# Kernel optimization log

Hardware: AMD Instinct MI355X
Metric: run time of the kernel (lower is better)

Reference implementation:

```python
import jax, jax.numpy as jnp
import numpy as np

N, K, D_IN, D_OUT = 50000, 32, 128, 128
TEMPERATURE = 1.0


def setup_inputs() -> dict:
    key = jax.random.key(0)
    k1, k2, k3 = jax.random.split(key, 3)
    feat = jax.random.normal(k1, (N, D_IN), dtype=jnp.float32)
    # Glorot-like scale so pairwise distances stay in a reasonable softmax range
    weight = jax.random.normal(k2, (D_IN, D_OUT), dtype=jnp.float32) / np.sqrt(D_IN)
    bias = jnp.zeros((D_OUT,), dtype=jnp.float32)
    # norm='none' -> unit edge weights; fixed-degree-k graph -> topk returns all k neighbors
    top_k_weights = jnp.ones((N, K), dtype=jnp.float32)
    top_k_idx = jax.random.randint(k3, (N, K), 0, N, dtype=jnp.int64)
    return {"feat": feat, "weight": weight, "bias": bias,
            "top_k_weights": top_k_weights, "top_k_idx": top_k_idx}


def reference(feat, weight, bias, top_k_weights, top_k_idx):
    # Linear projection (self.weight): [n, d_out]
    h = feat @ weight
    # Gather top-k neighbor embeddings: [n, k, d]
    fk = h[top_k_idx]
    mask = top_k_idx == -1                      # [n, k] missing-neighbor mask
    w = jnp.where(mask, 0.0, top_k_weights)     # zero out missing weights

    # Pairwise Euclidean distances among each node's k neighbors: [n, k, k]
    # ||a-b|| = sqrt(|a|^2 + |b|^2 - 2 a.b); avoids materializing [n,k,k,d]
    sq = jnp.sum(fk * fk, axis=-1)                          # [n, k]
    gram = jnp.einsum('nkd,nmd->nkm', fk, fk)               # [n, k, k]
    d2 = sq[:, :, None] + sq[:, None, :] - 2.0 * gram
    d2 = jnp.maximum(d2, 0.0)
    dist = jnp.sqrt(jnp.where(d2 > 0.0, d2, 1.0))
    dist = jnp.where(d2 > 0.0, dist, 0.0)                   # zero for identical pts / -1 idx
    # zero entries for missing pairs (matches partial_distance_matrix semantics)
    pair_mask = mask[:, :, None] | mask[:, None, :]
    dist = jnp.where(pair_mask, 0.0, dist)

    # Weighted sum of distances over neighbors (medoid cost): [n, k]
    dagg = jnp.einsum('nm,nkm->nk', w, dist)
    big = jnp.finfo(dist.dtype).max
    dagg = jnp.where(mask | ~jnp.isfinite(dagg), big, dagg)

    # Soft medoid weights
    r = jax.nn.softmax(-dagg / TEMPERATURE, axis=-1)
    # with_weight_correction=True
    r = r * w
    r = r / jnp.sum(r, axis=-1, keepdims=True)
    r = jnp.where(mask, 0.0, r)

    # spmm over the reliable adjacency: [n, d_out]
    out = jnp.einsum('nk,nkd->nd', r, fk)
    return out + bias
```

## Files before the change

kernel.cpp:

```cpp
#include <hip/hip_runtime.h>
#include <math.h>


typedef __attribute__((ext_vector_type(2)))  _Float16 half2v;
typedef __attribute__((ext_vector_type(4)))  _Float16 half4v;
typedef __attribute__((ext_vector_type(8)))  _Float16 half8;
typedef __attribute__((ext_vector_type(16))) float    f32x16;

#define NK   32
#define DIM  128
#define FKT_SZ 4224

__global__ __launch_bounds__(256) void prep(const float* __restrict__ W,
                                            _Float16* __restrict__ WT) {
    int t  = blockIdx.x * 256 + threadIdx.x;
    int nn = t >> 7, k = t & 127;
    WT[t] = (_Float16)W[k * 128 + nn];
}

__global__ __launch_bounds__(64) void gemm128(
    const float* __restrict__ A, const _Float16* __restrict__ WT,
    _Float16* __restrict__ Hq, int n)
{
    const int lane = threadIdx.x;
    const int l31  = lane & 31;
    const int hf   = lane >> 5;

    const int row  = blockIdx.x * 32 + l31;
    const int rowc = row < n ? row : n - 1;

    f32x16 acc[4];
#pragma unroll
    for (int t = 0; t < 4; ++t)
#pragma unroll
        for (int i = 0; i < 16; ++i) acc[t][i] = 0.0f;

    const float* ap = A + (size_t)rowc * 128 + 8 * hf;
#pragma unroll
    for (int s = 0; s < 8; ++s) {
        float4 b0 = *reinterpret_cast<const float4*>(ap + 16 * s);
        float4 b1 = *reinterpret_cast<const float4*>(ap + 16 * s + 4);
        half8 bf;
        bf[0] = (_Float16)b0.x; bf[1] = (_Float16)b0.y;
        bf[2] = (_Float16)b0.z; bf[3] = (_Float16)b0.w;
        bf[4] = (_Float16)b1.x; bf[5] = (_Float16)b1.y;
        bf[6] = (_Float16)b1.z; bf[7] = (_Float16)b1.w;
#pragma unroll
        for (int t = 0; t < 4; ++t) {
            half8 af = *reinterpret_cast<const half8*>(
                WT + (size_t)(l31 + 32 * t) * 128 + 16 * s + 8 * hf);
            acc[t] = __builtin_amdgcn_mfma_f32_32x32x16_f16(af, bf, acc[t], 0, 0, 0);
        }
    }

    if (row < n) {
        _Float16* hp = Hq + (size_t)row * 128;
#pragma unroll
        for (int t = 0; t < 4; ++t)
#pragma unroll
            for (int g = 0; g < 4; ++g) {
                half4v hv;
#pragma unroll
                for (int q = 0; q < 4; ++q) hv[q] = (_Float16)acc[t][4 * g + q];
                *reinterpret_cast<half4v*>(hp + 32 * t + 8 * g + 4 * hf) = hv;
            }
    }
}

__global__ __launch_bounds__(64, 4) void softk(
    const _Float16* __restrict__ hq, const float* __restrict__ bias,
    const float* __restrict__ tkw, const int* __restrict__ idx,
    float* __restrict__ out, int n)
{
    __shared__ __align__(16) _Float16 fkT[FKT_SZ];
    __shared__ __align__(16) float    rbuf[NK];

    const int lane = threadIdx.x;
    const int l31  = lane & 31;
    const int hf   = lane >> 5;
    const int pbase = (lane & 32) + ((lane & 32) >> 3);

    const int d0 = 2 * lane;
    const float2 bv = *reinterpret_cast<const float2*>(bias + d0);
    const _Float16* fb = &fkT[((d0 >> 3) * 33) * 8 + (d0 & 7)];
    const float4* rb = reinterpret_cast<const float4*>(&rbuf[0]);

    const int stride = gridDim.x;
    int nd = blockIdx.x;
    if (nd >= n) return;

    int   vid = idx[(size_t)nd * NK + l31];
    float tw  = tkw[(size_t)nd * NK + l31];
    int   mkc = (vid < 0) ? 1 : 0;
    float wc  = mkc ? 0.0f : tw;
    half8 frag[8];
    {
        const int idr = mkc ? 0 : vid;
        const half8* bp = reinterpret_cast<const half8*>(hq + (size_t)idr * DIM);
#pragma unroll
        for (int s = 0; s < 8; ++s) frag[s] = bp[2 * s + hf];
    }

    while (true) {
        const int  ndn = nd + stride;
        const bool hn  = ndn < n;

        int vid_n = 0; float tw_n = 0.0f;
        if (hn) {
            vid_n = idx[(size_t)ndn * NK + l31];
            tw_n  = tkw[(size_t)ndn * NK + l31];
        }

#pragma unroll
        for (int s = 0; s < 8; ++s) {
            int c = 2 * s + hf;
            *reinterpret_cast<half8*>(&fkT[(c * 33 + l31) * 8]) = frag[s];
        }

        f32x16 acc;
#pragma unroll
        for (int i = 0; i < 16; ++i) acc[i] = 0.0f;
#pragma unroll
        for (int s = 0; s < 8; ++s)
            acc = __builtin_amdgcn_mfma_f32_32x32x16_f16(frag[s], frag[s], acc, 0, 0, 0);

        float sqp = 0.0f;
#pragma unroll
        for (int s = 0; s < 8; ++s) {
            const half2v* p2 = reinterpret_cast<const half2v*>(&frag[s]);
#pragma unroll
            for (int q = 0; q < 4; ++q)
                sqp = __builtin_amdgcn_fdot2(p2[q], p2[q], sqp, false);
        }
        float sq = sqp + __shfl_xor(sqp, 32, 64);

        const int mk_n = (vid_n < 0) ? 1 : 0;
        half8 frag_n[8];
        if (hn) {
            const int idr_n = mk_n ? 0 : vid_n;
            const half8* bpn = reinterpret_cast<const half8*>(hq + (size_t)idr_n * DIM);
#pragma unroll
            for (int s = 0; s < 8; ++s) frag_n[s] = bpn[2 * s + hf];
        }

        {
            _Float16 shi = (_Float16)sq;
            _Float16 slo = (_Float16)(sq - (float)shi);
            _Float16 nh  = (_Float16)(-0.5f * (float)shi);
            _Float16 nl  = (_Float16)(-0.5f * (float)slo);
            _Float16 z   = (_Float16)0.0f, one = (_Float16)1.0f;
            half8 aext = {z, z, z, z, z, z, z, z};
            half8 bext = {z, z, z, z, z, z, z, z};
            if (hf == 0) {
                aext[0] = nh;  aext[1] = nl;  aext[2] = one; aext[3] = one;
                bext[0] = one; bext[1] = one; bext[2] = nh;  bext[3] = nl;
            }
            acc = __builtin_amdgcn_mfma_f32_32x32x16_f16(aext, bext, acc, 0, 0, 0);
        }

        float pt[4] = {0.0f, 0.0f, 0.0f, 0.0f};
#pragma unroll
        for (int reg = 0; reg < 16; ++reg) {
            const int c = (reg & 3) + 8 * (reg >> 2);
            float wr = __shfl(wc, pbase + c, 64);
            float d2 = fmaxf(-(acc[reg] + acc[reg]), 0.0f);
            float ds = (d2 > 1e-4f) ? __builtin_amdgcn_sqrtf(d2) : 0.0f;
            pt[reg & 3] = fmaf(wr, ds, pt[reg & 3]);
        }
        float part = (pt[0] + pt[1]) + (pt[2] + pt[3]);
        float sA = part + __shfl_xor(part, 32, 64);
        if (mkc || !(sA < 3.4028235e38f)) sA = 3.4028235e38f;

        float x  = -sA;
        float mx = x;
#pragma unroll
        for (int o = 16; o > 0; o >>= 1) mx = fmaxf(mx, __shfl_xor(mx, o, 32));
        float t  = __expf(x - mx) * wc;
        float st = t;
#pragma unroll
        for (int o = 16; o > 0; o >>= 1) st += __shfl_xor(st, o, 32);
        float r = t * __builtin_amdgcn_rcpf(st);

        rbuf[l31] = r;

        float o0 = 0.0f, o1 = 0.0f;
#pragma unroll
        for (int q = 0; q < 8; ++q) {
            float4 rv = rb[q];
            half2v h0 = *reinterpret_cast<const half2v*>(fb + 8 * (4 * q + 0));
            half2v h1 = *reinterpret_cast<const half2v*>(fb + 8 * (4 * q + 1));
            half2v h2 = *reinterpret_cast<const half2v*>(fb + 8 * (4 * q + 2));
            half2v h3 = *reinterpret_cast<const half2v*>(fb + 8 * (4 * q + 3));
            o0 = fmaf(rv.x, (float)h0[0], o0); o1 = fmaf(rv.x, (float)h0[1], o1);
            o0 = fmaf(rv.y, (float)h1[0], o0); o1 = fmaf(rv.y, (float)h1[1], o1);
            o0 = fmaf(rv.z, (float)h2[0], o0); o1 = fmaf(rv.z, (float)h2[1], o1);
            o0 = fmaf(rv.w, (float)h3[0], o0); o1 = fmaf(rv.w, (float)h3[1], o1);
        }
        float2 ov = { o0 + bv.x, o1 + bv.y };
        *reinterpret_cast<float2*>(out + (size_t)nd * DIM + d0) = ov;

        if (!hn) break;
        nd  = ndn;
        mkc = mk_n;
        wc  = mk_n ? 0.0f : tw_n;
#pragma unroll
        for (int s = 0; s < 8; ++s) frag[s] = frag_n[s];
    }
}

extern "C" void kernel_launch(void* const* d_in, const int* in_sizes, int n_in,
                              void* d_out, int out_size, void* d_ws, size_t ws_size,
                              hipStream_t stream) {
    const float* feat = (const float*)d_in[0];
    const float* W    = (const float*)d_in[1];
    const float* bias = (const float*)d_in[2];
    const float* tkw  = (const float*)d_in[3];
    const int*   idx  = (const int*)d_in[4];
    float* out = (float*)d_out;

    const int n = in_sizes[0] / DIM;
    _Float16* hq = (_Float16*)d_ws;
    _Float16* wt = hq + (size_t)n * DIM;

    const int gblocks = (n + 31) / 32;
    const int sblocks = (n + 3) / 4;

    prep<<<64, 256, 0, stream>>>(W, wt);
    gemm128<<<gblocks, 64, 0, stream>>>(feat, wt, hq, n);
    softk<<<sblocks, 64, 0, stream>>>(hq, bias, tkw, idx, out, n);
}
```

Measured before the change: 154.0 us.

## Coalesce neighbor-row gathers and stage fragments through swizzled LDS

Neighbor rows are now gathered so that 16 lanes read one contiguous 256-byte row of the projected features, instead of each lane fetching scattered 16-byte pieces of its own row. The rows are written to shared memory with a padded 272-byte stride and a rotating column swizzle. MFMA operands and the final weighted-sum operands are then read back from that shared buffer. The goal is fewer, wider global memory transactions in the gather-bound loop. The cost is extra LDS reads before the MFMAs and more involved address arithmetic.

```diff
diff --git a/kernel.cpp b/kernel.cpp
--- a/kernel.cpp
+++ b/kernel.cpp
@@ -9,7 +9,7 @@
 
 #define NK   32
 #define DIM  128
-#define FKT_SZ 4224
+#define ROWB 272
 
 __global__ __launch_bounds__(256) void prep(const float* __restrict__ W,
                                             _Float16* __restrict__ WT) {
@@ -72,18 +72,25 @@
     const float* __restrict__ tkw, const int* __restrict__ idx,
     float* __restrict__ out, int n)
 {
-    __shared__ __align__(16) _Float16 fkT[FKT_SZ];
-    __shared__ __align__(16) float    rbuf[NK];
+    __shared__ __align__(16) char  fkT[NK * ROWB];
+    __shared__ __align__(16) float rbuf[NK];
 
     const int lane = threadIdx.x;
     const int l31  = lane & 31;
     const int hf   = lane >> 5;
+    const int g    = lane >> 4;
+    const int m    = lane & 15;
     const int pbase = (lane & 32) + ((lane & 32) >> 3);
 
     const int d0 = 2 * lane;
     const float2 bv = *reinterpret_cast<const float2*>(bias + d0);
-    const _Float16* fb = &fkT[((d0 >> 3) * 33) * 8 + (d0 & 7)];
     const float4* rb = reinterpret_cast<const float4*>(&rbuf[0]);
+    const int wbase = ROWB * g + 16 * ((m + 4 * g) & 15);
+    const int fbase = ROWB * l31;
+    const int uc0   = 4 * hf + 16 * (l31 & 3);
+    int eaddr[4];
+#pragma unroll
+    for (int p = 0; p < 4; ++p) eaddr[p] = 4 * ((lane + 16 * p) & 63);
 
     const int stride = gridDim.x;
     int nd = blockIdx.x;
@@ -93,12 +100,15 @@
     float tw  = tkw[(size_t)nd * NK + l31];
     int   mkc = (vid < 0) ? 1 : 0;
     float wc  = mkc ? 0.0f : tw;
-    half8 frag[8];
+    half8 gb[8];
     {
-        const int idr = mkc ? 0 : vid;
-        const half8* bp = reinterpret_cast<const half8*>(hq + (size_t)idr * DIM);
-#pragma unroll
-        for (int s = 0; s < 8; ++s) frag[s] = bp[2 * s + hf];
+        int idr = mkc ? 0 : vid;
+#pragma unroll
+        for (int i = 0; i < 8; ++i) {
+            int idg = __shfl(idr, 4 * i + g, 64);
+            gb[i] = *reinterpret_cast<const half8*>(
+                hq + (size_t)idg * DIM + 8 * m);
+        }
     }
 
     while (true) {
@@ -112,22 +122,20 @@
         }
 
 #pragma unroll
+        for (int i = 0; i < 8; ++i)
+            *reinterpret_cast<half8*>(&fkT[1088 * i + wbase]) = gb[i];
+
+        f32x16 acc;
+#pragma unroll
+        for (int i = 0; i < 16; ++i) acc[i] = 0.0f;
+        float sqp = 0.0f;
+        int u = uc0;
+#pragma unroll
         for (int s = 0; s < 8; ++s) {
-            int c = 2 * s + hf;
-            *reinterpret_cast<half8*>(&fkT[(c * 33 + l31) * 8]) = frag[s];
-        }
-
-        f32x16 acc;
-#pragma unroll
-        for (int i = 0; i < 16; ++i) acc[i] = 0.0f;
-#pragma unroll
-        for (int s = 0; s < 8; ++s)
-            acc = __builtin_amdgcn_mfma_f32_32x32x16_f16(frag[s], frag[s], acc, 0, 0, 0);
-
-        float sqp = 0.0f;
-#pragma unroll
-        for (int s = 0; s < 8; ++s) {
-            const half2v* p2 = reinterpret_cast<const half2v*>(&frag[s]);
+            half8 fr = *reinterpret_cast<const half8*>(&fkT[fbase + 4 * (u & 63)]);
+            u += 8;
+            acc = __builtin_amdgcn_mfma_f32_32x32x16_f16(fr, fr, acc, 0, 0, 0);
+            const half2v* p2 = reinterpret_cast<const half2v*>(&fr);
 #pragma unroll
             for (int q = 0; q < 4; ++q)
                 sqp = __builtin_amdgcn_fdot2(p2[q], p2[q], sqp, false);
@@ -135,12 +143,15 @@
         float sq = sqp + __shfl_xor(sqp, 32, 64);
 
         const int mk_n = (vid_n < 0) ? 1 : 0;
-        half8 frag_n[8];
+        half8 gb_n[8];
         if (hn) {
-            const int idr_n = mk_n ? 0 : vid_n;
-            const half8* bpn = reinterpret_cast<const half8*>(hq + (size_t)idr_n * DIM);
-#pragma unroll
-            for (int s = 0; s < 8; ++s) frag_n[s] = bpn[2 * s + hf];
+            int idr_n = mk_n ? 0 : vid_n;
+#pragma unroll
+            for (int i = 0; i < 8; ++i) {
+                int idg = __shfl(idr_n, 4 * i + g, 64);
+                gb_n[i] = *reinterpret_cast<const half8*>(
+                    hq + (size_t)idg * DIM + 8 * m);
+            }
         }
 
         {
@@ -187,10 +198,10 @@
 #pragma unroll
         for (int q = 0; q < 8; ++q) {
             float4 rv = rb[q];
-            half2v h0 = *reinterpret_cast<const half2v*>(fb + 8 * (4 * q + 0));
-            half2v h1 = *reinterpret_cast<const half2v*>(fb + 8 * (4 * q + 1));
-            half2v h2 = *reinterpret_cast<const half2v*>(fb + 8 * (4 * q + 2));
-            half2v h3 = *reinterpret_cast<const half2v*>(fb + 8 * (4 * q + 3));
+            half2v h0 = *reinterpret_cast<const half2v*>(&fkT[ROWB * (4 * q + 0) + eaddr[0]]);
+            half2v h1 = *reinterpret_cast<const half2v*>(&fkT[ROWB * (4 * q + 1) + eaddr[1]]);
+            half2v h2 = *reinterpret_cast<const half2v*>(&fkT[ROWB * (4 * q + 2) + eaddr[2]]);
+            half2v h3 = *reinterpret_cast<const half2v*>(&fkT[ROWB * (4 * q + 3) + eaddr[3]]);
             o0 = fmaf(rv.x, (float)h0[0], o0); o1 = fmaf(rv.x, (float)h0[1], o1);
             o0 = fmaf(rv.y, (float)h1[0], o0); o1 = fmaf(rv.y, (float)h1[1], o1);
             o0 = fmaf(rv.z, (float)h2[0], o0); o1 = fmaf(rv.z, (float)h2[1], o1);
@@ -204,7 +215,7 @@
         mkc = mk_n;
         wc  = mk_n ? 0.0f : tw_n;
 #pragma unroll
-        for (int s = 0; s < 8; ++s) frag[s] = frag_n[s];
+        for (int i = 0; i < 8; ++i) gb[i] = gb_n[i];
     }
 }
 
```

Result: no change. 152.8 us (-0.8%).
